# Kernel tuning notes

Hardware: AMD Instinct MI355X
Metric: run time of the kernel (lower is better)

The kernel has to match this reference:

```python
import jax, jax.numpy as jnp
import numpy as np

# Mamba2 hyperparameters (from init_kwargs + mamba_ssm defaults)
D_MODEL = 1024
D_STATE = 64
D_CONV = 4
EXPAND = 2
HEADDIM = 64                      # mamba_ssm default
D_INNER = EXPAND * D_MODEL        # 2048
NHEADS = D_INNER // HEADDIM       # 32
NGROUPS = 1
CONV_DIM = D_INNER + 2 * NGROUPS * D_STATE      # 2176
D_IN_PROJ = 2 * D_INNER + 2 * NGROUPS * D_STATE + NHEADS  # 4256
BATCH, SEQLEN = 4, 2048


def setup_inputs() -> dict:
    key = jax.random.key(0)
    ks = jax.random.split(key, 8)
    x = jax.random.normal(ks[0], (BATCH, SEQLEN, D_MODEL), dtype=jnp.float32)
    W_in = jax.random.normal(ks[1], (D_MODEL, D_IN_PROJ), dtype=jnp.float32) * 0.02
    conv_w = jax.random.normal(ks[2], (CONV_DIM, D_CONV), dtype=jnp.float32) * 0.2
    conv_b = jnp.zeros((CONV_DIM,), dtype=jnp.float32)
    # dt_bias = inverse-softplus of dt ~ U(1e-3, 0.1), as in mamba_ssm init
    dt = jnp.exp(jax.random.uniform(ks[3], (NHEADS,)) * (np.log(0.1) - np.log(1e-3)) + np.log(1e-3))
    dt_bias = dt + jnp.log(-jnp.expm1(-dt))
    A_log = jnp.log(jax.random.uniform(ks[4], (NHEADS,), minval=1.0, maxval=16.0))
    D = jnp.ones((NHEADS,), dtype=jnp.float32)
    norm_w = jnp.ones((D_INNER,), dtype=jnp.float32)
    W_out = jax.random.normal(ks[5], (D_INNER, D_MODEL), dtype=jnp.float32) * 0.02
    return {"x": x, "W_in": W_in, "conv_w": conv_w, "conv_b": conv_b,
            "dt_bias": dt_bias, "A_log": A_log, "D": D, "norm_w": norm_w, "W_out": W_out}


def _mamba2_forward(x, W_in, conv_w, conv_b, dt_bias, A_log, D, norm_w, W_out):
    Bsz, L, _ = x.shape
    zxbcdt = x @ W_in                                   # [B, L, D_IN_PROJ]
    z = zxbcdt[..., :D_INNER]                           # gate
    xBC = zxbcdt[..., D_INNER:D_INNER + CONV_DIM]
    dt = zxbcdt[..., D_INNER + CONV_DIM:]               # [B, L, H]
    dt = jax.nn.softplus(dt + dt_bias)

    # causal depthwise conv1d over time, kernel width D_CONV
    xp = jnp.pad(xBC, ((0, 0), (D_CONV - 1, 0), (0, 0)))
    xc = sum(xp[:, k:k + L, :] * conv_w[:, k] for k in range(D_CONV))
    xBC = jax.nn.silu(xc + conv_b)

    xh = xBC[..., :D_INNER].reshape(Bsz, L, NHEADS, HEADDIM)   # [B,L,H,P]
    Bm = xBC[..., D_INNER:D_INNER + D_STATE]                   # [B,L,N] (ngroups=1)
    Cm = xBC[..., D_INNER + D_STATE:]                          # [B,L,N]
    A = -jnp.exp(A_log)                                        # [H]

    # selective SSM scan: h_t = h_{t-1}*exp(dt_t*A) + dt_t * x_t (outer) B_t ; y_t = C_t . h_t
    def step(h, inp):
        dt_t, x_t, B_t, C_t = inp                 # [B,H],[B,H,P],[B,N],[B,N]
        dA = jnp.exp(dt_t * A)                    # [B,H]
        h = h * dA[..., None, None] + (dt_t[..., None] * x_t)[..., None] * B_t[:, None, None, :]
        y_t = jnp.einsum('bhpn,bn->bhp', h, C_t)
        return h, y_t

    h0 = jnp.zeros((Bsz, NHEADS, HEADDIM, D_STATE), dtype=x.dtype)
    inputs = (jnp.moveaxis(dt, 1, 0), jnp.moveaxis(xh, 1, 0),
              jnp.moveaxis(Bm, 1, 0), jnp.moveaxis(Cm, 1, 0))
    _, ys = jax.lax.scan(step, h0, inputs)                     # [L,B,H,P]
    y = jnp.moveaxis(ys, 0, 1) + xh * D[None, None, :, None]   # skip term D*x
    y = y.reshape(Bsz, L, D_INNER)

    # gated RMSNorm: norm(y * silu(z)) * weight
    y = y * jax.nn.silu(z)
    y = y * jax.lax.rsqrt(jnp.mean(y * y, axis=-1, keepdims=True) + 1e-5) * norm_w
    return y @ W_out


def reference(x, W_in, conv_w, conv_b, dt_bias, A_log, D, norm_w, W_out):
    return _mamba2_forward(x, W_in, conv_w, conv_b, dt_bias, A_log, D, norm_w, W_out)
```

## Files before the change

kernel.cpp:

```cpp
#include <hip/hip_runtime.h>
#include <hip/hip_bf16.h>

#define B_SZ   4
#define SEQ    2048
#define DM     1024
#define DIN    2048
#define DST    64
#define NH     32
#define HD     64
#define CONVD  2176
#define DPROJ  4256
#define NPROJ  4224
#define MROWS  (B_SZ*SEQ)
#define QC     64
#define NC     (SEQ/QC)


typedef __attribute__((ext_vector_type(8))) __bf16 bf16x8;
typedef __attribute__((ext_vector_type(4))) __bf16 bf16x4;
typedef __attribute__((ext_vector_type(4))) float  floatx4;

__device__ __forceinline__ int swz(int row, int col) {
    return row * 64 + ((((col >> 3) ^ (row & 7)) << 3) | (col & 7));
}
__device__ __forceinline__ float bfbits2f(unsigned short u) {
    return __uint_as_float(((unsigned int)u) << 16);
}
__device__ __forceinline__ unsigned short f2bfbits(float f) {
    union { __bf16 h; unsigned short u; } cv; cv.h = (__bf16)f; return cv.u;
}

__global__ __launch_bounds__(256) void prep_weights_kernel(const float* __restrict__ W_in,
                                                           const float* __restrict__ W_out,
                                                           const float* __restrict__ norm_w,
                                                           float* __restrict__ dtWc,
                                                           __bf16* __restrict__ WinT,
                                                           __bf16* __restrict__ WoutT) {
    __shared__ float tile[32][129];
    const int bid = blockIdx.x, tid = threadIdx.x;
    if (bid < 128) {
        int idx = bid * 256 + tid;
        int k = idx >> 5, h = idx & 31;
        dtWc[idx] = W_in[(size_t)k * DPROJ + 2 * DIN + 2 * DST + h];
        return;
    }
    const float* src; __bf16* dst; const float* scal; int Ksrc, Csrc, mb, kb;
    if (bid < 128 + 1056) {
        int t = bid - 128; mb = t >> 5; kb = t & 31;
        src = W_in; dst = WinT; scal = nullptr; Ksrc = DM; Csrc = DPROJ;
    } else {
        int t = bid - 1184; mb = t >> 6; kb = t & 63;
        src = W_out; dst = WoutT; scal = norm_w; Ksrc = DIN; Csrc = DM;
    }
    const int K32 = Ksrc >> 5;
    #pragma unroll
    for (int i = 0; i < 4; i++) {
        int idx = tid + 256 * i;
        int kl = idx >> 5, c4 = idx & 31;
        int n = mb * 128 + c4 * 4;
        float4 v = make_float4(0.f, 0.f, 0.f, 0.f);
        if (n < Csrc) v = *(const float4*)(src + (size_t)(kb * 32 + kl) * Csrc + n);
        if (scal) { float s = scal[kb * 32 + kl]; v.x *= s; v.y *= s; v.z *= s; v.w *= s; }
        tile[kl][c4 * 4 + 0] = v.x; tile[kl][c4 * 4 + 1] = v.y;
        tile[kl][c4 * 4 + 2] = v.z; tile[kl][c4 * 4 + 3] = v.w;
    }
    __syncthreads();
    #pragma unroll
    for (int i = 0; i < 2; i++) {
        int c = tid + 256 * i;
        int sub = c >> 6, ln = c & 63, q = ln >> 4, lmn = ln & 15;
        bf16x8 o;
        #pragma unroll
        for (int e = 0; e < 8; e++) o[e] = (__bf16)tile[q * 8 + e][sub * 16 + lmn];
        *(bf16x8*)(dst + ((((size_t)(mb * 8 + sub)) * K32 + kb) << 9) + (ln << 3)) = o;
    }
}

__global__ __launch_bounds__(256) void cvt_dt_kernel(const float* __restrict__ x,
                                                     const float* __restrict__ dtWc,
                                                     __bf16* __restrict__ xbf,
                                                     float* __restrict__ dtraw) {
    __shared__ float xs[16][132];
    __shared__ float dtw[128 * 32];
    const int tid = threadIdx.x;
    const int r0 = blockIdx.x * 16;
    const int lm = tid & 15, pos = tid >> 4;
    const int rr = tid >> 4, h2 = (tid & 15) * 2;
    __bf16* slab = xbf + (size_t)blockIdx.x * (16 * DM);

    float a0 = 0.f, a1 = 0.f;
    for (int kc = 0; kc < 8; kc++) {
        #pragma unroll
        for (int i = 0; i < 2; i++) {
            int idx = tid + 256 * i;
            int row = idx >> 5, c4 = idx & 31;
            float4 v = ((const float4*)(x + (size_t)(r0 + row) * DM + kc * 128))[c4];
            xs[row][c4 * 4 + 0] = v.x; xs[row][c4 * 4 + 1] = v.y;
            xs[row][c4 * 4 + 2] = v.z; xs[row][c4 * 4 + 3] = v.w;
        }
        #pragma unroll
        for (int i = 0; i < 16; i++)
            dtw[tid + 256 * i] = dtWc[kc * 4096 + tid + 256 * i];
        __syncthreads();
        {
            bf16x8 o;
            #pragma unroll
            for (int e = 0; e < 8; e++) o[e] = (__bf16)xs[lm][pos * 8 + e];
            int kb = kc * 4 + (pos >> 2), q = pos & 3;
            *(bf16x8*)(slab + (size_t)(kb * 64 + q * 16 + lm) * 8) = o;
        }
        for (int j = 0; j < 128; j++) {
            float xv = xs[rr][j];
            a0 = fmaf(xv, dtw[j * 32 + h2], a0);
            a1 = fmaf(xv, dtw[j * 32 + h2 + 1], a1);
        }
        __syncthreads();
    }
    dtraw[(size_t)(r0 + rr) * NH + h2]     = a0;
    dtraw[(size_t)(r0 + rr) * NH + h2 + 1] = a1;
}

template<int STORE_BF16>
__global__ __launch_bounds__(256) void gemm_tt_kernel(const __bf16* __restrict__ A,
                                                      const __bf16* __restrict__ Bt,
                                                      float* __restrict__ Cf,
                                                      __bf16* __restrict__ Cb,
                                                      const float* __restrict__ rowscale,
                                                      int N, int K) {
    __shared__ __align__(16) __bf16 As[4096];
    __shared__ __align__(16) __bf16 Bs[4096];
    const int tid = threadIdx.x;
    const int wave = tid >> 6, lane = tid & 63;
    const int lm = lane & 15, lq = lane >> 4;
    const int mb = blockIdx.x, nb = blockIdx.y;
    const int K32 = K >> 5;

    floatx4 acc[4][4] = {};

    for (int kb = 0; kb < K32; kb++) {
        #pragma unroll
        for (int r = 0; r < 2; r++) {
            int c = tid + (r << 8);
            int sub = c >> 6, ln = c & 63;
            __builtin_amdgcn_global_load_lds(
                reinterpret_cast<const unsigned int*>(
                    A + ((((size_t)(mb * 8 + sub)) * K32 + kb) << 9) + (ln << 3)),
                reinterpret_cast<unsigned int*>(As + (size_t)c * 8), 16, 0, 0);
            __builtin_amdgcn_global_load_lds(
                reinterpret_cast<const unsigned int*>(
                    Bt + ((((size_t)(nb * 8 + sub)) * K32 + kb) << 9) + (ln << 3)),
                reinterpret_cast<unsigned int*>(Bs + (size_t)c * 8), 16, 0, 0);
        }
        __syncthreads();
        bf16x8 af[4], bfr[4];
        #pragma unroll
        for (int i = 0; i < 4; i++)
            af[i] = *(const bf16x8*)(As + ((((wave & 1) << 2) + i) << 9) + (lane << 3));
        #pragma unroll
        for (int i = 0; i < 4; i++)
            bfr[i] = *(const bf16x8*)(Bs + ((((wave >> 1) << 2) + i) << 9) + (lane << 3));
        #pragma unroll
        for (int mi = 0; mi < 4; mi++)
            #pragma unroll
            for (int ni = 0; ni < 4; ni++)
                acc[mi][ni] = __builtin_amdgcn_mfma_f32_16x16x32_bf16(af[mi], bfr[ni], acc[mi][ni], 0, 0, 0);
        __syncthreads();
    }

    const int wm = (wave & 1) << 6, wn = (wave >> 1) << 6;
    #pragma unroll
    for (int mi = 0; mi < 4; mi++) {
        #pragma unroll
        for (int r = 0; r < 4; r++) {
            int row = mb * 128 + wm + mi * 16 + lq * 4 + r;
            float s = 1.f;
            if (rowscale) s = rsqrtf(rowscale[row] * (1.f / (float)DIN) + 1e-5f);
            #pragma unroll
            for (int ni = 0; ni < 4; ni++) {
                int col = nb * 128 + wn + ni * 16 + lm;
                if (col < N) {
                    if (STORE_BF16) Cb[(size_t)row * N + col] = (__bf16)acc[mi][ni][r];
                    else            Cf[(size_t)row * N + col] = acc[mi][ni][r] * s;
                }
            }
        }
    }
}

__global__ __launch_bounds__(256) void conv_dt_kernel(const __bf16* __restrict__ zx,
                                                      const float* __restrict__ cw,
                                                      const float* __restrict__ cb,
                                                      __bf16* __restrict__ out,
                                                      const float* __restrict__ dtraw,
                                                      const float* __restrict__ dt_bias,
                                                      const float* __restrict__ A_log,
                                                      float* __restrict__ dtv,
                                                      float* __restrict__ cum,
                                                      float* __restrict__ rowsum) {
    const int bid = blockIdx.x, tid = threadIdx.x;
    if (bid < 1088) {
        const int by = bid / 17, bx = bid - by * 17;
        const int tc = tid & 15, tt = tid >> 4;
        const int c0 = (bx * 16 + tc) * 8;
        const int tg = by * 16 + tt;
        const int b = tg >> 8, t0 = (tg & 255) << 3;

        float xb[11][8];
        #pragma unroll
        for (int i = 0; i < 11; i++) {
            int t = t0 + i - 3;
            if (t >= 0) {
                bf16x8 v = *(const bf16x8*)(zx + ((size_t)(b * SEQ + t)) * NPROJ + DIN + c0);
                #pragma unroll
                for (int j = 0; j < 8; j++) xb[i][j] = (float)v[j];
            } else {
                #pragma unroll
                for (int j = 0; j < 8; j++) xb[i][j] = 0.f;
            }
        }
        float w0[8], w1[8], w2[8], w3[8], bias[8];
        #pragma unroll
        for (int j = 0; j < 8; j++) {
            float4 w = *(const float4*)(cw + (size_t)(c0 + j) * 4);
            w0[j] = w.x; w1[j] = w.y; w2[j] = w.z; w3[j] = w.w;
            bias[j] = cb[c0 + j];
        }
        #pragma unroll
        for (int s = 0; s < 8; s++) {
            bf16x8 o;
            #pragma unroll
            for (int j = 0; j < 8; j++) {
                float v = bias[j] + w0[j] * xb[s][j] + w1[j] * xb[s + 1][j]
                                  + w2[j] * xb[s + 2][j] + w3[j] * xb[s + 3][j];
                o[j] = (__bf16)(v / (1.f + __expf(-v)));
            }
            *(bf16x8*)(out + ((size_t)(b * SEQ + t0 + s)) * CONVD + c0) = o;
        }
    } else if (bid < 1216) {
        const int blk = bid - 1088;
        const int b = blk >> 5, h = blk & 31;
        const int wave = tid >> 6, lane = tid & 63;
        float Ah = -__expf(A_log[h]);
        float dtb = dt_bias[h];
        for (int c = wave; c < NC; c += 4) {
            int t = c * QC + lane;
            float u = dtraw[((size_t)b * SEQ + t) * NH + h] + dtb;
            float d = fmaxf(u, 0.f) + log1pf(__expf(-fabsf(u)));
            float s = d * Ah;
            #pragma unroll
            for (int o = 1; o < 64; o <<= 1) {
                float v = __shfl_up(s, o);
                if (lane >= o) s += v;
            }
            size_t idx = (size_t)blk * SEQ + t;
            dtv[idx] = d;
            cum[idx] = s;
        }
    } else {
        float4 z = make_float4(0.f, 0.f, 0.f, 0.f);
        *(float4*)(rowsum + (size_t)(bid - 1216) * 1024 + tid * 4) = z;
    }
}

__global__ __launch_bounds__(256) void chunk_state_kernel(const __bf16* __restrict__ xc,
                                                          const float* __restrict__ dtv,
                                                          const float* __restrict__ cum,
                                                          __bf16* __restrict__ Sbuf) {
    const int blk = blockIdx.x;
    const int hq = blk & 7;
    const int bc = blk >> 3;
    const int c = bc & (NC - 1), b = bc >> 5;
    const int tid = threadIdx.x;
    const int wave = tid >> 6, lane = tid & 63;
    const int lm = lane & 15, q = lane >> 4;
    const int h = hq * 4 + wave;

    __shared__ __align__(16) __bf16 sBt[4096];
    __shared__ __align__(16) __bf16 sXw[4][4096];

    const size_t rowbase = (size_t)b * SEQ + (size_t)c * QC;
    {
        int k = tid & 31, n0 = (tid >> 5) * 8;
        unsigned short u0[8], u1[8];
        *(uint4*)u0 = *(const uint4*)(xc + (rowbase + 2 * k) * CONVD + DIN + n0);
        *(uint4*)u1 = *(const uint4*)(xc + (rowbase + 2 * k + 1) * CONVD + DIN + n0);
        #pragma unroll
        for (int i = 0; i < 8; i++) {
            unsigned int v = (unsigned int)u0[i] | ((unsigned int)u1[i] << 16);
            ((unsigned int*)sBt)[swz(n0 + i, 2 * k) >> 1] = v;
        }
    }
    const float* cump = cum + (size_t)(b * NH + h) * SEQ + (size_t)c * QC;
    const float* dtp  = dtv + (size_t)(b * NH + h) * SEQ + (size_t)c * QC;
    {
        int k = lane & 31, ph = (lane >> 5) * 32;
        float clast = cump[63];
        float w0 = dtp[2 * k]     * __expf(clast - cump[2 * k]);
        float w1 = dtp[2 * k + 1] * __expf(clast - cump[2 * k + 1]);
        unsigned short u0[32], u1[32];
        const __bf16* r0 = xc + (rowbase + 2 * k) * CONVD + h * 64 + ph;
        const __bf16* r1 = xc + (rowbase + 2 * k + 1) * CONVD + h * 64 + ph;
        #pragma unroll
        for (int i = 0; i < 4; i++) {
            ((uint4*)u0)[i] = ((const uint4*)r0)[i];
            ((uint4*)u1)[i] = ((const uint4*)r1)[i];
        }
        unsigned int* dstw = (unsigned int*)sXw[wave];
        #pragma unroll
        for (int i = 0; i < 32; i++) {
            unsigned int lo = f2bfbits(bfbits2f(u0[i]) * w0);
            unsigned int hi = f2bfbits(bfbits2f(u1[i]) * w1);
            dstw[swz(ph + i, 2 * k) >> 1] = lo | (hi << 16);
        }
    }
    __syncthreads();

    floatx4 acc[4][4] = {};
    #pragma unroll
    for (int kb = 0; kb < 2; kb++) {
        bf16x8 aX[4], bB[4];
        #pragma unroll
        for (int pi = 0; pi < 4; pi++)
            aX[pi] = *(const bf16x8*)(&sXw[wave][swz(pi * 16 + lm, kb * 32 + q * 8)]);
        #pragma unroll
        for (int ni = 0; ni < 4; ni++)
            bB[ni] = *(const bf16x8*)(&sBt[swz(ni * 16 + lm, kb * 32 + q * 8)]);
        #pragma unroll
        for (int pi = 0; pi < 4; pi++)
            #pragma unroll
            for (int ni = 0; ni < 4; ni++)
                acc[pi][ni] = __builtin_amdgcn_mfma_f32_16x16x32_bf16(aX[pi], bB[ni], acc[pi][ni], 0, 0, 0);
    }
    __bf16* Sp = Sbuf + ((size_t)(b * NC + c) * NH + h) * (HD * DST);
    #pragma unroll
    for (int pi = 0; pi < 4; pi++)
        #pragma unroll
        for (int r = 0; r < 4; r++) {
            int p = pi * 16 + q * 4 + r;
            #pragma unroll
            for (int ni = 0; ni < 4; ni++)
                Sp[p * 64 + ni * 16 + lm] = (__bf16)acc[pi][ni][r];
        }
}

__global__ __launch_bounds__(256) void state_scan_kernel(__bf16* __restrict__ Sbuf,
                                                         const float* __restrict__ cum) {
    int blk = blockIdx.x >> 2;
    int part = blockIdx.x & 3;
    int b = blk >> 5, h = blk & 31;
    int off = part * 1024 + threadIdx.x * 4;
    float run[4];
    #pragma unroll
    for (int n = 0; n < 4; n++) run[n] = 0.f;
    for (int c = 0; c < NC; c++) {
        __bf16* Sp = Sbuf + ((size_t)(b * NC + c) * NH + h) * (HD * DST) + off;
        bf16x4 sv = *(const bf16x4*)Sp;
        float tmp[4];
        #pragma unroll
        for (int n = 0; n < 4; n++) tmp[n] = (float)sv[n];
        bf16x4 ov;
        #pragma unroll
        for (int n = 0; n < 4; n++) ov[n] = (__bf16)run[n];
        *(bf16x4*)Sp = ov;
        float P = __expf(cum[(size_t)blk * SEQ + c * QC + QC - 1]);
        #pragma unroll
        for (int n = 0; n < 4; n++) run[n] = fmaf(run[n], P, tmp[n]);
    }
}

__global__ __launch_bounds__(128) void chunk_out_kernel(const __bf16* __restrict__ xc,
                                                        const float* __restrict__ dtv,
                                                        const float* __restrict__ cum,
                                                        const __bf16* __restrict__ Sbuf,
                                                        const float* __restrict__ Dv,
                                                        const __bf16* __restrict__ zx,
                                                        float* __restrict__ rowsum,
                                                        __bf16* __restrict__ y) {
    const int blk = blockIdx.x;
    const int hp = blk & 15;
    const int bc = blk >> 4;
    const int c = bc & (NC - 1), b = bc >> 5;
    const int tid = threadIdx.x;
    const int wave = tid >> 6, lane = tid & 63;
    const int lm = lane & 15, q = lane >> 4;
    const int h = hp * 2 + wave;

    __shared__ __align__(16) __bf16 smem[16384];
    __bf16* sB  = smem;
    __bf16* sC  = smem + 4096;
    __bf16* sXt = smem + 8192 + (wave << 12);
    __bf16* sP  = smem + (wave << 12);

    const size_t rowbase = (size_t)b * SEQ + (size_t)c * QC;
    {
        int r = tid >> 1, c0 = (tid & 1) * 32;
        const __bf16* gB = xc + (rowbase + r) * CONVD + DIN + c0;
        const __bf16* gC = xc + (rowbase + r) * CONVD + DIN + DST + c0;
        #pragma unroll
        for (int i = 0; i < 4; i++) {
            *(uint4*)(&sB[swz(r, c0 + i * 8)]) = *(const uint4*)(gB + i * 8);
            *(uint4*)(&sC[swz(r, c0 + i * 8)]) = *(const uint4*)(gC + i * 8);
        }
    }
    {
        int k = lane & 31, ph = (lane >> 5) * 32;
        unsigned short u0[32], u1[32];
        const __bf16* r0 = xc + (rowbase + 2 * k) * CONVD + h * 64 + ph;
        const __bf16* r1 = xc + (rowbase + 2 * k + 1) * CONVD + h * 64 + ph;
        #pragma unroll
        for (int i = 0; i < 4; i++) {
            ((uint4*)u0)[i] = ((const uint4*)r0)[i];
            ((uint4*)u1)[i] = ((const uint4*)r1)[i];
        }
        unsigned int* dstw = (unsigned int*)sXt;
        #pragma unroll
        for (int i = 0; i < 32; i++)
            dstw[swz(ph + i, 2 * k) >> 1] = (unsigned int)u0[i] | ((unsigned int)u1[i] << 16);
    }
    __syncthreads();

    const float* cump = cum + (size_t)(b * NH + h) * SEQ + (size_t)c * QC;
    const float* dtp  = dtv + (size_t)(b * NH + h) * SEQ + (size_t)c * QC;
    float cumv = cump[lane], dtvv = dtp[lane];
    float ct[4][4];
    #pragma unroll
    for (int ti = 0; ti < 4; ti++)
        #pragma unroll
        for (int r = 0; r < 4; r++)
            ct[ti][r] = __shfl(cumv, ti * 16 + q * 4 + r);
    float cums_l[4], dtv_l[4];
    #pragma unroll
    for (int si = 0; si < 4; si++) {
        cums_l[si] = __shfl(cumv, si * 16 + lm);
        dtv_l[si]  = __shfl(dtvv, si * 16 + lm);
    }

    bf16x8 afC[4][2];
    #pragma unroll
    for (int ti = 0; ti < 4; ti++)
        #pragma unroll
        for (int kb = 0; kb < 2; kb++)
            afC[ti][kb] = *(const bf16x8*)(&sC[swz(ti * 16 + lm, kb * 32 + q * 8)]);

    floatx4 accG[4][4] = {};
    #pragma unroll
    for (int kb = 0; kb < 2; kb++) {
        bf16x8 bfB[4];
        #pragma unroll
        for (int si = 0; si < 4; si++)
            bfB[si] = *(const bf16x8*)(&sB[swz(si * 16 + lm, kb * 32 + q * 8)]);
        #pragma unroll
        for (int ti = 0; ti < 4; ti++)
            #pragma unroll
            for (int si = 0; si < 4; si++)
                if (si <= ti)
                    accG[ti][si] = __builtin_amdgcn_mfma_f32_16x16x32_bf16(afC[ti][kb], bfB[si], accG[ti][si], 0, 0, 0);
    }
    __syncthreads();

    float Dh = Dv[h];
    #pragma unroll
    for (int ti = 0; ti < 4; ti++)
        #pragma unroll
        for (int si = 0; si < 4; si++) {
            if (si > ti) continue;
            #pragma unroll
            for (int r = 0; r < 4; r++) {
                int t = ti * 16 + q * 4 + r;
                float arg = fminf(ct[ti][r] - cums_l[si], 0.f);
                float val = dtv_l[si] * __expf(arg) * accG[ti][si][r];
                if (ti == si) {
                    if (lm > q * 4 + r) val = 0.f;
                    else if (lm == q * 4 + r) val += Dh;
                }
                sP[swz(t, si * 16 + lm)] = (__bf16)val;
            }
        }
    #pragma unroll
    for (int r = 0; r < 4; r++) {
        sP[swz(q * 4 + r, 16 + lm)] = (__bf16)0.f;
        sP[swz(32 + q * 4 + r, 48 + lm)] = (__bf16)0.f;
    }
    __syncthreads();

    floatx4 accY[4][4] = {};
    const __bf16* Sp = Sbuf + ((size_t)(b * NC + c) * NH + h) * (HD * DST);
    #pragma unroll
    for (int kb = 0; kb < 2; kb++) {
        bf16x8 bS[4];
        #pragma unroll
        for (int pi = 0; pi < 4; pi++)
            bS[pi] = *(const bf16x8*)(Sp + (pi * 16 + lm) * 64 + kb * 32 + q * 8);
        #pragma unroll
        for (int ti = 0; ti < 4; ti++)
            #pragma unroll
            for (int pi = 0; pi < 4; pi++)
                accY[ti][pi] = __builtin_amdgcn_mfma_f32_16x16x32_bf16(afC[ti][kb], bS[pi], accY[ti][pi], 0, 0, 0);
    }
    #pragma unroll
    for (int ti = 0; ti < 4; ti++)
        #pragma unroll
        for (int r = 0; r < 4; r++) {
            float e = __expf(ct[ti][r]);
            #pragma unroll
            for (int pi = 0; pi < 4; pi++)
                accY[ti][pi][r] *= e;
        }

    #pragma unroll
    for (int kb = 0; kb < 2; kb++) {
        bf16x8 bX[4];
        #pragma unroll
        for (int pi = 0; pi < 4; pi++)
            bX[pi] = *(const bf16x8*)(&sXt[swz(pi * 16 + lm, kb * 32 + q * 8)]);
        #pragma unroll
        for (int ti = 0; ti < 4; ti++) {
            if (ti < 2 * kb) continue;
            bf16x8 aP = *(const bf16x8*)(&sP[swz(ti * 16 + lm, kb * 32 + q * 8)]);
            #pragma unroll
            for (int pi = 0; pi < 4; pi++)
                accY[ti][pi] = __builtin_amdgcn_mfma_f32_16x16x32_bf16(aP, bX[pi], accY[ti][pi], 0, 0, 0);
        }
    }

    const int R4v = (int)(rowbase >> 4);
    #pragma unroll
    for (int ti = 0; ti < 4; ti++) {
        __bf16* slab = y + (size_t)(R4v + ti) * 32768;
        #pragma unroll
        for (int r = 0; r < 4; r++) {
            int t = ti * 16 + q * 4 + r;
            const __bf16* zrow = zx + (rowbase + t) * NPROJ + h * 64;
            float rs = 0.f;
            #pragma unroll
            for (int pi = 0; pi < 4; pi++) {
                float zv = (float)zrow[pi * 16 + lm];
                float g = accY[ti][pi][r] * (zv / (1.f + __expf(-zv)));
                rs += g * g;
                int kbC = h * 2 + (pi >> 1);
                int qC  = ((pi & 1) << 1) + (lm >> 3);
                slab[kbC * 512 + qC * 128 + (lm & 7) + (q * 4 + r) * 8] = (__bf16)g;
            }
            rs += __shfl_xor(rs, 1);
            rs += __shfl_xor(rs, 2);
            rs += __shfl_xor(rs, 4);
            rs += __shfl_xor(rs, 8);
            if (lm == 0) atomicAdd(&rowsum[rowbase + t], rs);
        }
    }
}

extern "C" void kernel_launch(void* const* d_in, const int* in_sizes, int n_in,
                              void* d_out, int out_size, void* d_ws, size_t ws_size,
                              hipStream_t stream) {
    const float* x       = (const float*)d_in[0];
    const float* W_in    = (const float*)d_in[1];
    const float* conv_w  = (const float*)d_in[2];
    const float* conv_b  = (const float*)d_in[3];
    const float* dt_bias = (const float*)d_in[4];
    const float* A_log   = (const float*)d_in[5];
    const float* Dv      = (const float*)d_in[6];
    const float* norm_w  = (const float*)d_in[7];
    const float* W_out   = (const float*)d_in[8];
    float* out = (float*)d_out;

    char* ws = (char*)d_ws;
    size_t off = 0;
    auto take = [&](size_t bytes) { void* p = ws + off; off = (off + bytes + 255) & ~(size_t)255; return p; };
    __bf16* xbf    = (__bf16*)take((size_t)MROWS * DM * 2);
    __bf16* WinT   = (__bf16*)take((size_t)NPROJ * DM * 2);
    __bf16* WoutT  = (__bf16*)take((size_t)DM * DIN * 2);
    __bf16* zx     = (__bf16*)take((size_t)MROWS * NPROJ * 2);
    __bf16* xc     = (__bf16*)take((size_t)MROWS * CONVD * 2);
    __bf16* yf     = (__bf16*)take((size_t)MROWS * DIN * 2);
    float*  dtraw  = (float*) take((size_t)MROWS * NH * 4);
    float*  dtv    = (float*) take((size_t)B_SZ * NH * SEQ * 4);
    float*  cum    = (float*) take((size_t)B_SZ * NH * SEQ * 4);
    __bf16* Sbuf   = (__bf16*)take((size_t)B_SZ * NC * NH * HD * DST * 2);
    float*  dtWc   = (float*) take((size_t)DM * NH * 4);
    float*  rowsum = (float*) take((size_t)MROWS * 4);
    (void)ws_size;

    prep_weights_kernel<<<dim3(1696), 256, 0, stream>>>(W_in, W_out, norm_w, dtWc, WinT, WoutT);
    cvt_dt_kernel<<<dim3(MROWS / 16), 256, 0, stream>>>(x, dtWc, xbf, dtraw);
    gemm_tt_kernel<1><<<dim3(MROWS / 128, NPROJ / 128), 256, 0, stream>>>(
        xbf, WinT, nullptr, zx, nullptr, NPROJ, DM);
    conv_dt_kernel<<<dim3(1224), 256, 0, stream>>>(zx, conv_w, conv_b, xc,
                                                   dtraw, dt_bias, A_log, dtv, cum, rowsum);
    chunk_state_kernel<<<dim3(B_SZ * NC * (NH / 4)), 256, 0, stream>>>(xc, dtv, cum, Sbuf);
    state_scan_kernel<<<dim3(B_SZ * NH * 4), 256, 0, stream>>>(Sbuf, cum);
    chunk_out_kernel<<<dim3(B_SZ * NC * (NH / 2)), 128, 0, stream>>>(
        xc, dtv, cum, Sbuf, Dv, zx, rowsum, yf);
    gemm_tt_kernel<0><<<dim3(MROWS / 128, DM / 128), 256, 0, stream>>>(
        yf, WoutT, out, nullptr, rowsum, DM, DIN);
}
```

Before: 379.6 us.

## Fuse causal conv into chunk kernels and merge prep/cvt and dt-scan into GEMM launch

Removes the standalone conv kernel and its xc intermediate buffer. The depthwise conv plus SiLU is recomputed on the fly from the projection output inside chunk_state and chunk_out. The weight prep and x conversion kernels are merged into one launch that reads dt weights straight from W_in. The dt cumsum and rowsum-zeroing blocks are appended to the first GEMM launch. This cuts kernel launches and the global write and read of xc, at the cost of redundant conv recompute and more register pressure in the chunk kernels.

```diff
diff --git a/kernel.cpp b/kernel.cpp
--- a/kernel.cpp
+++ b/kernel.cpp
@@ -8,7 +8,6 @@
 #define DST    64
 #define NH     32
 #define HD     64
-#define CONVD  2176
 #define DPROJ  4256
 #define NPROJ  4224
 #define MROWS  (B_SZ*SEQ)
@@ -26,67 +25,59 @@
 __device__ __forceinline__ float bfbits2f(unsigned short u) {
     return __uint_as_float(((unsigned int)u) << 16);
 }
-__device__ __forceinline__ unsigned short f2bfbits(float f) {
-    union { __bf16 h; unsigned short u; } cv; cv.h = (__bf16)f; return cv.u;
-}
-
-__global__ __launch_bounds__(256) void prep_weights_kernel(const float* __restrict__ W_in,
-                                                           const float* __restrict__ W_out,
-                                                           const float* __restrict__ norm_w,
-                                                           float* __restrict__ dtWc,
-                                                           __bf16* __restrict__ WinT,
-                                                           __bf16* __restrict__ WoutT) {
-    __shared__ float tile[32][129];
+__device__ __forceinline__ float silu_f(float v) { return v / (1.f + __expf(-v)); }
+
+__global__ __launch_bounds__(256) void prep_cvt_kernel(const float* __restrict__ x,
+                                                       const float* __restrict__ W_in,
+                                                       const float* __restrict__ W_out,
+                                                       const float* __restrict__ norm_w,
+                                                       __bf16* __restrict__ xbf,
+                                                       __bf16* __restrict__ WinT,
+                                                       __bf16* __restrict__ WoutT,
+                                                       float* __restrict__ dtraw) {
+    __shared__ float smem[16 * 132 + 4096];
     const int bid = blockIdx.x, tid = threadIdx.x;
-    if (bid < 128) {
-        int idx = bid * 256 + tid;
-        int k = idx >> 5, h = idx & 31;
-        dtWc[idx] = W_in[(size_t)k * DPROJ + 2 * DIN + 2 * DST + h];
+    if (bid < 1568) {
+        float (*tile)[129] = (float (*)[129])smem;
+        const float* src; __bf16* dst; const float* scal; int Ksrc, Csrc, mb, kb;
+        if (bid < 1056) {
+            mb = bid >> 5; kb = bid & 31;
+            src = W_in; dst = WinT; scal = nullptr; Ksrc = DM; Csrc = DPROJ;
+        } else {
+            int t = bid - 1056; mb = t >> 6; kb = t & 63;
+            src = W_out; dst = WoutT; scal = norm_w; Ksrc = DIN; Csrc = DM;
+        }
+        const int K32 = Ksrc >> 5;
+        #pragma unroll
+        for (int i = 0; i < 4; i++) {
+            int idx = tid + 256 * i;
+            int kl = idx >> 5, c4 = idx & 31;
+            int n = mb * 128 + c4 * 4;
+            float4 v = make_float4(0.f, 0.f, 0.f, 0.f);
+            if (n < Csrc) v = *(const float4*)(src + (size_t)(kb * 32 + kl) * Csrc + n);
+            if (scal) { float s = scal[kb * 32 + kl]; v.x *= s; v.y *= s; v.z *= s; v.w *= s; }
+            tile[kl][c4 * 4 + 0] = v.x; tile[kl][c4 * 4 + 1] = v.y;
+            tile[kl][c4 * 4 + 2] = v.z; tile[kl][c4 * 4 + 3] = v.w;
+        }
+        __syncthreads();
+        #pragma unroll
+        for (int i = 0; i < 2; i++) {
+            int c = tid + 256 * i;
+            int sub = c >> 6, ln = c & 63, q = ln >> 4, lmn = ln & 15;
+            bf16x8 o;
+            #pragma unroll
+            for (int e = 0; e < 8; e++) o[e] = (__bf16)tile[q * 8 + e][sub * 16 + lmn];
+            *(bf16x8*)(dst + ((((size_t)(mb * 8 + sub)) * K32 + kb) << 9) + (ln << 3)) = o;
+        }
         return;
     }
-    const float* src; __bf16* dst; const float* scal; int Ksrc, Csrc, mb, kb;
-    if (bid < 128 + 1056) {
-        int t = bid - 128; mb = t >> 5; kb = t & 31;
-        src = W_in; dst = WinT; scal = nullptr; Ksrc = DM; Csrc = DPROJ;
-    } else {
-        int t = bid - 1184; mb = t >> 6; kb = t & 63;
-        src = W_out; dst = WoutT; scal = norm_w; Ksrc = DIN; Csrc = DM;
-    }
-    const int K32 = Ksrc >> 5;
-    #pragma unroll
-    for (int i = 0; i < 4; i++) {
-        int idx = tid + 256 * i;
-        int kl = idx >> 5, c4 = idx & 31;
-        int n = mb * 128 + c4 * 4;
-        float4 v = make_float4(0.f, 0.f, 0.f, 0.f);
-        if (n < Csrc) v = *(const float4*)(src + (size_t)(kb * 32 + kl) * Csrc + n);
-        if (scal) { float s = scal[kb * 32 + kl]; v.x *= s; v.y *= s; v.z *= s; v.w *= s; }
-        tile[kl][c4 * 4 + 0] = v.x; tile[kl][c4 * 4 + 1] = v.y;
-        tile[kl][c4 * 4 + 2] = v.z; tile[kl][c4 * 4 + 3] = v.w;
-    }
-    __syncthreads();
-    #pragma unroll
-    for (int i = 0; i < 2; i++) {
-        int c = tid + 256 * i;
-        int sub = c >> 6, ln = c & 63, q = ln >> 4, lmn = ln & 15;
-        bf16x8 o;
-        #pragma unroll
-        for (int e = 0; e < 8; e++) o[e] = (__bf16)tile[q * 8 + e][sub * 16 + lmn];
-        *(bf16x8*)(dst + ((((size_t)(mb * 8 + sub)) * K32 + kb) << 9) + (ln << 3)) = o;
-    }
-}
-
-__global__ __launch_bounds__(256) void cvt_dt_kernel(const float* __restrict__ x,
-                                                     const float* __restrict__ dtWc,
-                                                     __bf16* __restrict__ xbf,
-                                                     float* __restrict__ dtraw) {
-    __shared__ float xs[16][132];
-    __shared__ float dtw[128 * 32];
-    const int tid = threadIdx.x;
-    const int r0 = blockIdx.x * 16;
+    float (*xs)[132] = (float (*)[132])smem;
+    float* dtw = smem + 16 * 132;
+    const int slabi = bid - 1568;
+    const int r0 = slabi * 16;
     const int lm = tid & 15, pos = tid >> 4;
     const int rr = tid >> 4, h2 = (tid & 15) * 2;
-    __bf16* slab = xbf + (size_t)blockIdx.x * (16 * DM);
+    __bf16* slab = xbf + (size_t)slabi * (16 * DM);
 
     float a0 = 0.f, a1 = 0.f;
     for (int kc = 0; kc < 8; kc++) {
@@ -99,8 +90,10 @@
             xs[row][c4 * 4 + 2] = v.z; xs[row][c4 * 4 + 3] = v.w;
         }
         #pragma unroll
-        for (int i = 0; i < 16; i++)
-            dtw[tid + 256 * i] = dtWc[kc * 4096 + tid + 256 * i];
+        for (int i = 0; i < 16; i++) {
+            int idx = tid + 256 * i;
+            dtw[idx] = W_in[(size_t)(kc * 128 + (idx >> 5)) * DPROJ + NPROJ + (idx & 31)];
+        }
         __syncthreads();
         {
             bf16x8 o;
@@ -121,18 +114,17 @@
 }
 
 template<int STORE_BF16>
-__global__ __launch_bounds__(256) void gemm_tt_kernel(const __bf16* __restrict__ A,
-                                                      const __bf16* __restrict__ Bt,
-                                                      float* __restrict__ Cf,
-                                                      __bf16* __restrict__ Cb,
-                                                      const float* __restrict__ rowscale,
-                                                      int N, int K) {
+__device__ __forceinline__ void gemm_body(const __bf16* __restrict__ A,
+                                          const __bf16* __restrict__ Bt,
+                                          float* __restrict__ Cf,
+                                          __bf16* __restrict__ Cb,
+                                          const float* __restrict__ rowscale,
+                                          int N, int K, int mb, int nb) {
     __shared__ __align__(16) __bf16 As[4096];
     __shared__ __align__(16) __bf16 Bs[4096];
     const int tid = threadIdx.x;
     const int wave = tid >> 6, lane = tid & 63;
     const int lm = lane & 15, lq = lane >> 4;
-    const int mb = blockIdx.x, nb = blockIdx.y;
     const int K32 = K >> 5;
 
     floatx4 acc[4][4] = {};
@@ -187,57 +179,20 @@
     }
 }
 
-__global__ __launch_bounds__(256) void conv_dt_kernel(const __bf16* __restrict__ zx,
-                                                      const float* __restrict__ cw,
-                                                      const float* __restrict__ cb,
-                                                      __bf16* __restrict__ out,
-                                                      const float* __restrict__ dtraw,
-                                                      const float* __restrict__ dt_bias,
-                                                      const float* __restrict__ A_log,
-                                                      float* __restrict__ dtv,
-                                                      float* __restrict__ cum,
-                                                      float* __restrict__ rowsum) {
+__global__ __launch_bounds__(256) void gemm1_kernel(const __bf16* __restrict__ A,
+                                                    const __bf16* __restrict__ Bt,
+                                                    __bf16* __restrict__ Cb,
+                                                    const float* __restrict__ dtraw,
+                                                    const float* __restrict__ dt_bias,
+                                                    const float* __restrict__ A_log,
+                                                    float* __restrict__ dtv,
+                                                    float* __restrict__ cum,
+                                                    float* __restrict__ rowsum) {
     const int bid = blockIdx.x, tid = threadIdx.x;
-    if (bid < 1088) {
-        const int by = bid / 17, bx = bid - by * 17;
-        const int tc = tid & 15, tt = tid >> 4;
-        const int c0 = (bx * 16 + tc) * 8;
-        const int tg = by * 16 + tt;
-        const int b = tg >> 8, t0 = (tg & 255) << 3;
-
-        float xb[11][8];
-        #pragma unroll
-        for (int i = 0; i < 11; i++) {
-            int t = t0 + i - 3;
-            if (t >= 0) {
-                bf16x8 v = *(const bf16x8*)(zx + ((size_t)(b * SEQ + t)) * NPROJ + DIN + c0);
-                #pragma unroll
-                for (int j = 0; j < 8; j++) xb[i][j] = (float)v[j];
-            } else {
-                #pragma unroll
-                for (int j = 0; j < 8; j++) xb[i][j] = 0.f;
-            }
-        }
-        float w0[8], w1[8], w2[8], w3[8], bias[8];
-        #pragma unroll
-        for (int j = 0; j < 8; j++) {
-            float4 w = *(const float4*)(cw + (size_t)(c0 + j) * 4);
-            w0[j] = w.x; w1[j] = w.y; w2[j] = w.z; w3[j] = w.w;
-            bias[j] = cb[c0 + j];
-        }
-        #pragma unroll
-        for (int s = 0; s < 8; s++) {
-            bf16x8 o;
-            #pragma unroll
-            for (int j = 0; j < 8; j++) {
-                float v = bias[j] + w0[j] * xb[s][j] + w1[j] * xb[s + 1][j]
-                                  + w2[j] * xb[s + 2][j] + w3[j] * xb[s + 3][j];
-                o[j] = (__bf16)(v / (1.f + __expf(-v)));
-            }
-            *(bf16x8*)(out + ((size_t)(b * SEQ + t0 + s)) * CONVD + c0) = o;
-        }
-    } else if (bid < 1216) {
-        const int blk = bid - 1088;
+    if (bid < 2112) {
+        gemm_body<1>(A, Bt, nullptr, Cb, nullptr, NPROJ, DM, bid & 63, bid >> 6);
+    } else if (bid < 2240) {
+        const int blk = bid - 2112;
         const int b = blk >> 5, h = blk & 31;
         const int wave = tid >> 6, lane = tid & 63;
         float Ah = -__expf(A_log[h]);
@@ -258,11 +213,20 @@
         }
     } else {
         float4 z = make_float4(0.f, 0.f, 0.f, 0.f);
-        *(float4*)(rowsum + (size_t)(bid - 1216) * 1024 + tid * 4) = z;
-    }
-}
-
-__global__ __launch_bounds__(256) void chunk_state_kernel(const __bf16* __restrict__ xc,
+        *(float4*)(rowsum + (size_t)(bid - 2240) * 1024 + tid * 4) = z;
+    }
+}
+
+__global__ __launch_bounds__(256) void gemm2_kernel(const __bf16* __restrict__ A,
+                                                    const __bf16* __restrict__ Bt,
+                                                    float* __restrict__ Cf,
+                                                    const float* __restrict__ rowscale) {
+    gemm_body<0>(A, Bt, Cf, nullptr, rowscale, DM, DIN, blockIdx.x, blockIdx.y);
+}
+
+__global__ __launch_bounds__(256) void chunk_state_kernel(const __bf16* __restrict__ zx,
+                                                          const float* __restrict__ cw,
+                                                          const float* __restrict__ cb,
                                                           const float* __restrict__ dtv,
                                                           const float* __restrict__ cum,
                                                           __bf16* __restrict__ Sbuf) {
@@ -278,39 +242,80 @@
     __shared__ __align__(16) __bf16 sBt[4096];
     __shared__ __align__(16) __bf16 sXw[4][4096];
 
-    const size_t rowbase = (size_t)b * SEQ + (size_t)c * QC;
+    const __bf16* zb = zx + (size_t)b * SEQ * NPROJ;
     {
-        int k = tid & 31, n0 = (tid >> 5) * 8;
-        unsigned short u0[8], u1[8];
-        *(uint4*)u0 = *(const uint4*)(xc + (rowbase + 2 * k) * CONVD + DIN + n0);
-        *(uint4*)u1 = *(const uint4*)(xc + (rowbase + 2 * k + 1) * CONVD + DIN + n0);
-        #pragma unroll
-        for (int i = 0; i < 8; i++) {
-            unsigned int v = (unsigned int)u0[i] | ((unsigned int)u1[i] << 16);
-            ((unsigned int*)sBt)[swz(n0 + i, 2 * k) >> 1] = v;
-        }
+        const int rg = tid >> 5, cs = tid & 31;
+        const int n0 = 2 * cs;
+        float4 wA = *(const float4*)(cw + (size_t)(2048 + n0) * 4);
+        float  bA = cb[2048 + n0];
+        float4 wB = *(const float4*)(cw + (size_t)(2048 + n0 + 1) * 4);
+        float  bB = cb[2048 + n0 + 1];
+        unsigned int rv[11];
+        const int tbase = c * QC + rg * 8 - 3;
+        #pragma unroll
+        for (int i = 0; i < 11; i++) {
+            int t = tbase + i;
+            rv[i] = (t >= 0) ? *(const unsigned int*)(zb + (size_t)t * NPROJ + 4096 + n0) : 0u;
+        }
+        bf16x8 olo, ohi;
+        #pragma unroll
+        for (int sl = 0; sl < 8; sl++) {
+            float xl[4], xh[4];
+            #pragma unroll
+            for (int k = 0; k < 4; k++) {
+                unsigned int u = rv[sl + k];
+                xl[k] = bfbits2f((unsigned short)(u & 0xffff));
+                xh[k] = bfbits2f((unsigned short)(u >> 16));
+            }
+            olo[sl] = (__bf16)silu_f(bA + wA.x*xl[0] + wA.y*xl[1] + wA.z*xl[2] + wA.w*xl[3]);
+            ohi[sl] = (__bf16)silu_f(bB + wB.x*xh[0] + wB.y*xh[1] + wB.z*xh[2] + wB.w*xh[3]);
+        }
+        *(bf16x8*)&sBt[swz(n0,     rg * 8)] = olo;
+        *(bf16x8*)&sBt[swz(n0 + 1, rg * 8)] = ohi;
     }
     const float* cump = cum + (size_t)(b * NH + h) * SEQ + (size_t)c * QC;
     const float* dtp  = dtv + (size_t)(b * NH + h) * SEQ + (size_t)c * QC;
     {
-        int k = lane & 31, ph = (lane >> 5) * 32;
+        const int cg = lane >> 3, rg = lane & 7;
+        const int jx = h * 64 + cg * 8;
+        float w4[8][4], bs[8];
+        #pragma unroll
+        for (int e = 0; e < 8; e++) {
+            float4 w = *(const float4*)(cw + (size_t)(jx + e) * 4);
+            w4[e][0] = w.x; w4[e][1] = w.y; w4[e][2] = w.z; w4[e][3] = w.w;
+            bs[e] = cb[jx + e];
+        }
+        float rf[11][8];
+        const int tbase = c * QC + rg * 8 - 3;
+        #pragma unroll
+        for (int i = 0; i < 11; i++) {
+            int t = tbase + i;
+            if (t >= 0) {
+                bf16x8 v = *(const bf16x8*)(zb + (size_t)t * NPROJ + 2048 + jx);
+                #pragma unroll
+                for (int e = 0; e < 8; e++) rf[i][e] = (float)v[e];
+            } else {
+                #pragma unroll
+                for (int e = 0; e < 8; e++) rf[i][e] = 0.f;
+            }
+        }
         float clast = cump[63];
-        float w0 = dtp[2 * k]     * __expf(clast - cump[2 * k]);
-        float w1 = dtp[2 * k + 1] * __expf(clast - cump[2 * k + 1]);
-        unsigned short u0[32], u1[32];
-        const __bf16* r0 = xc + (rowbase + 2 * k) * CONVD + h * 64 + ph;
-        const __bf16* r1 = xc + (rowbase + 2 * k + 1) * CONVD + h * 64 + ph;
-        #pragma unroll
-        for (int i = 0; i < 4; i++) {
-            ((uint4*)u0)[i] = ((const uint4*)r0)[i];
-            ((uint4*)u1)[i] = ((const uint4*)r1)[i];
-        }
-        unsigned int* dstw = (unsigned int*)sXw[wave];
-        #pragma unroll
-        for (int i = 0; i < 32; i++) {
-            unsigned int lo = f2bfbits(bfbits2f(u0[i]) * w0);
-            unsigned int hi = f2bfbits(bfbits2f(u1[i]) * w1);
-            dstw[swz(ph + i, 2 * k) >> 1] = lo | (hi << 16);
+        float wdt[8];
+        #pragma unroll
+        for (int sl = 0; sl < 8; sl++) {
+            int s = rg * 8 + sl;
+            wdt[sl] = dtp[s] * __expf(clast - cump[s]);
+        }
+        #pragma unroll
+        for (int e = 0; e < 8; e++) {
+            bf16x8 o;
+            #pragma unroll
+            for (int sl = 0; sl < 8; sl++) {
+                float v = bs[e] + w4[e][0]*rf[sl][e] + w4[e][1]*rf[sl+1][e]
+                                + w4[e][2]*rf[sl+2][e] + w4[e][3]*rf[sl+3][e];
+                o[sl] = (__bf16)(silu_f(v) * wdt[sl]);
+            }
+            *(bf16x8*)&sXw[wave][swz(cg * 8 + e, rg * 8)] = o;
         }
     }
     __syncthreads();
@@ -368,12 +373,13 @@
     }
 }
 
-__global__ __launch_bounds__(128) void chunk_out_kernel(const __bf16* __restrict__ xc,
+__global__ __launch_bounds__(128) void chunk_out_kernel(const __bf16* __restrict__ zx,
+                                                        const float* __restrict__ cw,
+                                                        const float* __restrict__ cb,
                                                         const float* __restrict__ dtv,
                                                         const float* __restrict__ cum,
                                                         const __bf16* __restrict__ Sbuf,
                                                         const float* __restrict__ Dv,
-                                                        const __bf16* __restrict__ zx,
                                                         float* __restrict__ rowsum,
                                                         __bf16* __restrict__ y) {
     const int blk = blockIdx.x;
@@ -391,31 +397,80 @@
     __bf16* sXt = smem + 8192 + (wave << 12);
     __bf16* sP  = smem + (wave << 12);
 
+    const __bf16* zb = zx + (size_t)b * SEQ * NPROJ;
     const size_t rowbase = (size_t)b * SEQ + (size_t)c * QC;
     {
-        int r = tid >> 1, c0 = (tid & 1) * 32;
-        const __bf16* gB = xc + (rowbase + r) * CONVD + DIN + c0;
-        const __bf16* gC = xc + (rowbase + r) * CONVD + DIN + DST + c0;
-        #pragma unroll
-        for (int i = 0; i < 4; i++) {
-            *(uint4*)(&sB[swz(r, c0 + i * 8)]) = *(const uint4*)(gB + i * 8);
-            *(uint4*)(&sC[swz(r, c0 + i * 8)]) = *(const uint4*)(gC + i * 8);
+        const int cg = lane >> 3, rg = lane & 7;
+        const int jx = 2048 + wave * 64 + cg * 8;
+        __bf16* sDst = wave ? sC : sB;
+        float w4[8][4], bs[8];
+        #pragma unroll
+        for (int e = 0; e < 8; e++) {
+            float4 w = *(const float4*)(cw + (size_t)(jx + e) * 4);
+            w4[e][0] = w.x; w4[e][1] = w.y; w4[e][2] = w.z; w4[e][3] = w.w;
+            bs[e] = cb[jx + e];
+        }
+        float rf[11][8];
+        const int tbase = c * QC + rg * 8 - 3;
+        #pragma unroll
+        for (int i = 0; i < 11; i++) {
+            int t = tbase + i;
+            if (t >= 0) {
+                bf16x8 v = *(const bf16x8*)(zb + (size_t)t * NPROJ + 2048 + jx);
+                #pragma unroll
+                for (int e = 0; e < 8; e++) rf[i][e] = (float)v[e];
+            } else {
+                #pragma unroll
+                for (int e = 0; e < 8; e++) rf[i][e] = 0.f;
+            }
+        }
+        #pragma unroll
+        for (int sl = 0; sl < 8; sl++) {
+            bf16x8 o;
+            #pragma unroll
+            for (int e = 0; e < 8; e++) {
+                float v = bs[e] + w4[e][0]*rf[sl][e] + w4[e][1]*rf[sl+1][e]
+                                + w4[e][2]*rf[sl+2][e] + w4[e][3]*rf[sl+3][e];
+                o[e] = (__bf16)silu_f(v);
+            }
+            *(bf16x8*)&sDst[swz(rg * 8 + sl, cg * 8)] = o;
         }
     }
     {
-        int k = lane & 31, ph = (lane >> 5) * 32;
-        unsigned short u0[32], u1[32];
-        const __bf16* r0 = xc + (rowbase + 2 * k) * CONVD + h * 64 + ph;
-        const __bf16* r1 = xc + (rowbase + 2 * k + 1) * CONVD + h * 64 + ph;
-        #pragma unroll
-        for (int i = 0; i < 4; i++) {
-            ((uint4*)u0)[i] = ((const uint4*)r0)[i];
-            ((uint4*)u1)[i] = ((const uint4*)r1)[i];
-        }
-        unsigned int* dstw = (unsigned int*)sXt;
-        #pragma unroll
-        for (int i = 0; i < 32; i++)
-            dstw[swz(ph + i, 2 * k) >> 1] = (unsigned int)u0[i] | ((unsigned int)u1[i] << 16);
+        const int cg = lane >> 3, rg = lane & 7;
+        const int jx = h * 64 + cg * 8;
+        float w4[8][4], bs[8];
+        #pragma unroll
+        for (int e = 0; e < 8; e++) {
+            float4 w = *(const float4*)(cw + (size_t)(jx + e) * 4);
+            w4[e][0] = w.x; w4[e][1] = w.y; w4[e][2] = w.z; w4[e][3] = w.w;
+            bs[e] = cb[jx + e];
+        }
+        float rf[11][8];
+        const int tbase = c * QC + rg * 8 - 3;
+        #pragma unroll
+        for (int i = 0; i < 11; i++) {
+            int t = tbase + i;
+            if (t >= 0) {
+                bf16x8 v = *(const bf16x8*)(zb + (size_t)t * NPROJ + 2048 + jx);
+                #pragma unroll
+                for (int e = 0; e < 8; e++) rf[i][e] = (float)v[e];
+            } else {
+                #pragma unroll
+                for (int e = 0; e < 8; e++) rf[i][e] = 0.f;
+            }
+        }
+        #pragma unroll
+        for (int e = 0; e < 8; e++) {
+            bf16x8 o;
+            #pragma unroll
+            for (int sl = 0; sl < 8; sl++) {
+                float v = bs[e] + w4[e][0]*rf[sl][e] + w4[e][1]*rf[sl+1][e]
+                                + w4[e][2]*rf[sl+2][e] + w4[e][3]*rf[sl+3][e];
+                o[sl] = (__bf16)silu_f(v);
+            }
+            *(bf16x8*)&sXt[swz(cg * 8 + e, rg * 8)] = o;
+        }
     }
     __syncthreads();
 
@@ -535,7 +590,7 @@
             #pragma unroll
             for (int pi = 0; pi < 4; pi++) {
                 float zv = (float)zrow[pi * 16 + lm];
-                float g = accY[ti][pi][r] * (zv / (1.f + __expf(-zv)));
+                float g = accY[ti][pi][r] * silu_f(zv);
                 rs += g * g;
                 int kbC = h * 2 + (pi >> 1);
                 int qC  = ((pi & 1) << 1) + (lm >> 3);
@@ -571,26 +626,22 @@
     __bf16* WinT   = (__bf16*)take((size_t)NPROJ * DM * 2);
     __bf16* WoutT  = (__bf16*)take((size_t)DM * DIN * 2);
     __bf16* zx     = (__bf16*)take((size_t)MROWS * NPROJ * 2);
-    __bf16* xc     = (__bf16*)take((size_t)MROWS * CONVD * 2);
     __bf16* yf     = (__bf16*)take((size_t)MROWS * DIN * 2);
     float*  dtraw  = (float*) take((size_t)MROWS * NH * 4);
     float*  dtv    = (float*) take((size_t)B_SZ * NH * SEQ * 4);
     float*  cum    = (float*) take((size_t)B_SZ * NH * SEQ * 4);
     __bf16* Sbuf   = (__bf16*)take((size_t)B_SZ * NC * NH * HD * DST * 2);
-    float*  dtWc   = (float*) take((size_t)DM * NH * 4);
     float*  rowsum = (float*) take((size_t)MROWS * 4);
     (void)ws_size;
 
-    prep_weights_kernel<<<dim3(1696), 256, 0, stream>>>(W_in, W_out, norm_w, dtWc, WinT, WoutT);
-    cvt_dt_kernel<<<dim3(MROWS / 16), 256, 0, stream>>>(x, dtWc, xbf, dtraw);
-    gemm_tt_kernel<1><<<dim3(MROWS / 128, NPROJ / 128), 256, 0, stream>>>(
-        xbf, WinT, nullptr, zx, nullptr, NPROJ, DM);
-    conv_dt_kernel<<<dim3(1224), 256, 0, stream>>>(zx, conv_w, conv_b, xc,
-                                                   dtraw, dt_bias, A_log, dtv, cum, rowsum);
-    chunk_state_kernel<<<dim3(B_SZ * NC * (NH / 4)), 256, 0, stream>>>(xc, dtv, cum, Sbuf);
+    prep_cvt_kernel<<<dim3(2080), 256, 0, stream>>>(x, W_in, W_out, norm_w,
+                                                    xbf, WinT, WoutT, dtraw);
+    gemm1_kernel<<<dim3(2248), 256, 0, stream>>>(xbf, WinT, zx,
+                                                 dtraw, dt_bias, A_log, dtv, cum, rowsum);
+    chunk_state_kernel<<<dim3(B_SZ * NC * (NH / 4)), 256, 0, stream>>>(
+        zx, conv_w, conv_b, dtv, cum, Sbuf);
     state_scan_kernel<<<dim3(B_SZ * NH * 4), 256, 0, stream>>>(Sbuf, cum);
     chunk_out_kernel<<<dim3(B_SZ * NC * (NH / 2)), 128, 0, stream>>>(
-        xc, dtv, cum, Sbuf, Dv, zx, rowsum, yf);
-    gemm_tt_kernel<0><<<dim3(MROWS / 128, DM / 128), 256, 0, stream>>>(
-        yf, WoutT, out, nullptr, rowsum, DM, DIN);
-}
+        zx, conv_w, conv_b, dtv, cum, Sbuf, Dv, rowsum, yf);
+    gemm2_kernel<<<dim3(MROWS / 128, DM / 128), 256, 0, stream>>>(yf, WoutT, out, rowsum);
+}
```

After: 390.1 us. 2.8% more time.
